# Optimization experiments

Measured on AMD Instinct MI355X. Metric: run time of the kernel, lower is better.

The kernel has to match this reference:

```python
import math
import jax, jax.numpy as jnp
import numpy as np

B, T, O, C, H, L, V = 4, 1024, 128, 512, 8, 6, 32000
HD = C // H
PAD_ID = 0
EPS = 1e-6  # flax LayerNorm default


def _logit(p):
    p = float(min(max(p, 1e-06), 1.0 - 1e-06))
    return math.log(p / (1.0 - p))


def _ln(x, scale, bias):
    m = jnp.mean(x, axis=-1, keepdims=True)
    v = jnp.mean(jnp.square(x - m), axis=-1, keepdims=True)
    return (x - m) * jax.lax.rsqrt(v + EPS) * scale + bias


def _rope(x, fc):
    b, t, h, d = x.shape
    xc = jax.lax.complex(x[..., 0::2], x[..., 1::2])
    xr = xc * fc
    return jnp.stack([xr.real, xr.imag], axis=-1).reshape(b, t, h, d)


def _freqs_cis(dim, max_len, theta=10000.0):
    freqs = 1.0 / theta ** (jnp.arange(0, dim, 2) / dim)
    t = jnp.arange(max_len)
    return jnp.exp(1j * jnp.outer(t, freqs))[None, :, None, :]


def setup_inputs() -> dict:
    key = jax.random.key(0)
    ks = iter(jax.random.split(key, 64))
    def w(shape, s=0.02):
        return jax.random.normal(next(ks), shape, jnp.float32) * s
    inp = {
        'tokens_w': jax.random.randint(next(ks), (B, T), 0, V, dtype=jnp.int32),
        'mem': w((B, O, C), 1.0),
        'ssum': w((B, C), 1.0),
        'embed': w((V, C)),
        'mem_adapter_w': w((C, C)), 'mem_adapter_b': jnp.zeros((C,), jnp.float32),
        'mem_norm_scale': jnp.ones((C,), jnp.float32), 'mem_norm_bias': jnp.zeros((C,), jnp.float32),
        'alpha_gate': jnp.full((C,), _logit(0.1), jnp.float32),
        'lambda_gate': jnp.full((C,), _logit(0.9), jnp.float32),
        'ssum_proj_w': w((C, C)),
        'ln1_scale': jnp.ones((L, C), jnp.float32), 'ln1_bias': jnp.zeros((L, C), jnp.float32),
        'lnkv_scale': jnp.ones((L, C), jnp.float32), 'lnkv_bias': jnp.zeros((L, C), jnp.float32),
        'q_w': w((L, C, C)), 'q_b': jnp.zeros((L, C), jnp.float32),
        'k_w': w((L, C, C)), 'k_b': jnp.zeros((L, C), jnp.float32),
        'v_w': w((L, C, C)), 'v_b': jnp.zeros((L, C), jnp.float32),
        'o_w': w((L, C, C)), 'o_b': jnp.zeros((L, C), jnp.float32),
        'ln2_scale': jnp.ones((L, C), jnp.float32), 'ln2_bias': jnp.zeros((L, C), jnp.float32),
        'mlp_w1': w((L, C, 4 * C)), 'mlp_b1': jnp.zeros((L, 4 * C), jnp.float32),
        'mlp_w2': w((L, 4 * C, C)), 'mlp_b2': jnp.zeros((L, C), jnp.float32),
        'final_ln_scale': jnp.ones((C,), jnp.float32), 'final_ln_bias': jnp.zeros((C,), jnp.float32),
        'out_w': w((C, V)), 'out_b': jnp.zeros((V,), jnp.float32),
    }
    return inp


def reference(tokens_w, mem, ssum, embed, mem_adapter_w, mem_adapter_b,
              mem_norm_scale, mem_norm_bias, alpha_gate, lambda_gate, ssum_proj_w,
              ln1_scale, ln1_bias, lnkv_scale, lnkv_bias,
              q_w, q_b, k_w, k_b, v_w, v_b, o_w, o_b,
              ln2_scale, ln2_bias, mlp_w1, mlp_b1, mlp_w2, mlp_b2,
              final_ln_scale, final_ln_bias, out_w, out_b):
    x = embed[tokens_w]  # [B,T,C]
    mem_p = _ln(mem @ mem_adapter_w + mem_adapter_b, mem_norm_scale, mem_norm_bias)  # [B,O,C]
    alpha = jax.nn.sigmoid(alpha_gate)
    x = x + (ssum @ ssum_proj_w)[:, None, :] * alpha[None, None, :]

    causal = jnp.tril(jnp.ones((T, T), bool))
    full_mask = jnp.concatenate([jnp.ones((T, O), bool), causal], axis=1)  # [T,T+O]
    valid_curr = tokens_w != PAD_ID
    valid_k = jnp.concatenate([jnp.ones((B, O), bool), valid_curr], axis=1)  # [B,T+O]
    mask = full_mask[None, None, :, :] & valid_k[:, None, None, :]  # [B,1,T,T+O]

    fc = _freqs_cis(HD, T + O + 10)
    f_q = fc[:, -T:, :, :]
    f_k = fc[:, -(T + O):, :, :]
    scale = 1.0 / math.sqrt(HD)

    cur = x
    for i in range(L):
        nx = _ln(cur, ln1_scale[i], ln1_bias[i])
        kv = jnp.concatenate([mem_p, cur], axis=1)  # [B,T+O,C]
        nkv = _ln(kv, lnkv_scale[i], lnkv_bias[i])
        q = (nx @ q_w[i] + q_b[i]).reshape(B, T, H, HD)
        k = (nkv @ k_w[i] + k_b[i]).reshape(B, T + O, H, HD)
        v = (nkv @ v_w[i] + v_b[i]).reshape(B, T + O, H, HD)
        q = _rope(q, f_q)
        k = _rope(k, f_k)
        scores = jnp.einsum('bqhd,bkhd->bhqk', q, k) * scale
        scores = jnp.where(mask, scores, -1e9)
        probs = jax.nn.softmax(scores, axis=-1)
        attn = jnp.einsum('bhqk,bkhd->bqhd', probs, v).reshape(B, T, C)
        cur = cur + attn @ o_w[i] + o_b[i]
        h = _ln(cur, ln2_scale[i], ln2_bias[i])
        h = jax.nn.gelu(h @ mlp_w1[i] + mlp_b1[i]) @ mlp_w2[i] + mlp_b2[i]
        cur = cur + h

    cur = _ln(cur, final_ln_scale, final_ln_bias)
    new_mem = cur[:, -O:, :]
    out_mask = valid_curr.astype(jnp.float32)[:, :, None]
    masked = cur * out_mask
    logits = masked @ out_w + out_b
    win_sum = jnp.sum(masked, axis=1) / (jnp.sum(out_mask, axis=1) + 1e-6)
    lam = jax.nn.sigmoid(lambda_gate)
    new_ssum = ssum * lam[None, :] + win_sum * (1.0 - lam[None, :])
    return (new_mem, new_ssum, logits)
```

## Files before the change

### kernel.cpp

```cpp
#include <hip/hip_runtime.h>
#include <math.h>

#define NB 4
#define NT 1024
#define NO 128
#define NC 512
#define NH 8
#define NL 6
#define NV 32000
#define NHD 64
#define NTK (NT + NO)
#define NFF (4 * NC)

__device__ __forceinline__ float sigmoidf_(float x) { return 1.f / (1.f + __expf(-x)); }
__device__ __forceinline__ float gelu_(float x) {
    const float k0 = 0.7978845608028654f;
    float x3 = x * x * x;
    return 0.5f * x * (1.f + tanhf(k0 * (x + 0.044715f * x3)));
}

template <int ACT>
__global__ __launch_bounds__(256) void gemm_kernel(
    const float* __restrict__ A, const float* __restrict__ W,
    const float* __restrict__ bias, const float* __restrict__ res,
    float* __restrict__ out, int M, int N, int K)
{
    __shared__ float As[16][65];
    __shared__ float Bs[16][65];
    int tid = threadIdx.x;
    int bm = blockIdx.y * 64, bn = blockIdx.x * 64;
    int tx = tid & 15, ty = tid >> 4;
    float acc[4][4];
#pragma unroll
    for (int i = 0; i < 4; i++)
#pragma unroll
        for (int j = 0; j < 4; j++) acc[i][j] = 0.f;

    for (int k0 = 0; k0 < K; k0 += 16) {
        int ak = tid & 15, am = tid >> 4;
#pragma unroll
        for (int r = 0; r < 4; r++) {
            int m = am + r * 16;
            int gm = bm + m;
            As[ak][m] = (gm < M) ? A[(size_t)gm * K + k0 + ak] : 0.f;
        }
        int wn = tid & 63, wk = tid >> 6;
#pragma unroll
        for (int r = 0; r < 4; r++) {
            int kk = wk + r * 4;
            Bs[kk][wn] = W[(size_t)(k0 + kk) * N + bn + wn];
        }
        __syncthreads();
#pragma unroll
        for (int kk = 0; kk < 16; kk++) {
            float a[4], b[4];
#pragma unroll
            for (int i = 0; i < 4; i++) a[i] = As[kk][ty * 4 + i];
#pragma unroll
            for (int j = 0; j < 4; j++) b[j] = Bs[kk][tx * 4 + j];
#pragma unroll
            for (int i = 0; i < 4; i++)
#pragma unroll
                for (int j = 0; j < 4; j++) acc[i][j] = fmaf(a[i], b[j], acc[i][j]);
        }
        __syncthreads();
    }

#pragma unroll
    for (int i = 0; i < 4; i++) {
        int gm = bm + ty * 4 + i;
        if (gm >= M) continue;
#pragma unroll
        for (int j = 0; j < 4; j++) {
            int gn = bn + tx * 4 + j;
            float v = acc[i][j];
            if (bias) v += bias[gn];
            if (ACT == 1) v = gelu_(v);
            if (res) v += res[(size_t)gm * N + gn];
            out[(size_t)gm * N + gn] = v;
        }
    }
}

__global__ __launch_bounds__(256) void ln_kernel(
    const float* __restrict__ x, float* __restrict__ y,
    const float* __restrict__ scale, const float* __restrict__ bias)
{
    int row = blockIdx.x, tid = threadIdx.x;
    const float* xr = x + (size_t)row * NC;
    float v0 = xr[tid], v1 = xr[tid + 256];
    __shared__ float red[256];
    red[tid] = v0 + v1;
    __syncthreads();
    for (int s = 128; s > 0; s >>= 1) { if (tid < s) red[tid] += red[tid + s]; __syncthreads(); }
    float mean = red[0] * (1.f / NC);
    __syncthreads();
    float d0 = v0 - mean, d1 = v1 - mean;
    red[tid] = d0 * d0 + d1 * d1;
    __syncthreads();
    for (int s = 128; s > 0; s >>= 1) { if (tid < s) red[tid] += red[tid + s]; __syncthreads(); }
    float rs = rsqrtf(red[0] * (1.f / NC) + 1e-6f);
    float* yr = y + (size_t)row * NC;
    yr[tid] = d0 * rs * scale[tid] + bias[tid];
    yr[tid + 256] = d1 * rs * scale[tid + 256] + bias[tid + 256];
}

__global__ __launch_bounds__(256) void lnkv_kernel(
    const float* __restrict__ mem_p, const float* __restrict__ cur,
    float* __restrict__ y, const float* __restrict__ scale, const float* __restrict__ bias)
{
    int row = blockIdx.x;
    int b = row / NTK, r = row % NTK;
    const float* xr = (r < NO) ? (mem_p + (size_t)(b * NO + r) * NC)
                               : (cur + (size_t)(b * NT + (r - NO)) * NC);
    int tid = threadIdx.x;
    float v0 = xr[tid], v1 = xr[tid + 256];
    __shared__ float red[256];
    red[tid] = v0 + v1;
    __syncthreads();
    for (int s = 128; s > 0; s >>= 1) { if (tid < s) red[tid] += red[tid + s]; __syncthreads(); }
    float mean = red[0] * (1.f / NC);
    __syncthreads();
    float d0 = v0 - mean, d1 = v1 - mean;
    red[tid] = d0 * d0 + d1 * d1;
    __syncthreads();
    for (int s = 128; s > 0; s >>= 1) { if (tid < s) red[tid] += red[tid + s]; __syncthreads(); }
    float rs = rsqrtf(red[0] * (1.f / NC) + 1e-6f);
    float* yr = y + (size_t)row * NC;
    yr[tid] = d0 * rs * scale[tid] + bias[tid];
    yr[tid + 256] = d1 * rs * scale[tid + 256] + bias[tid + 256];
}

__global__ __launch_bounds__(256) void embed_kernel(
    const int* __restrict__ tokens, const float* __restrict__ emb,
    const float* __restrict__ sp, const float* __restrict__ alpha_gate,
    float* __restrict__ cur)
{
    int idx = blockIdx.x * 256 + threadIdx.x;
    int c = idx & (NC - 1);
    int t = (idx >> 9) & (NT - 1);
    int b = idx >> 19;
    int tok = tokens[b * NT + t];
    float a = sigmoidf_(alpha_gate[c]);
    cur[idx] = emb[(size_t)tok * NC + c] + sp[b * NC + c] * a;
}

__global__ __launch_bounds__(256) void rope_kernel(float* __restrict__ x, int rows, int pos_off)
{
    int idx = blockIdx.x * 256 + threadIdx.x;
    int total = NB * rows * NH * 32;
    if (idx >= total) return;
    int j = idx & 31;
    int h = (idx >> 5) & 7;
    int r = (idx >> 8) % rows;
    int b = (idx >> 8) / rows;
    double freq = exp(-(2.0 * j / 64.0) * log(10000.0));
    double ang = (double)(r + pos_off) * freq;
    double sd, cd;
    sincos(ang, &sd, &cd);
    float s = (float)sd, c = (float)cd;
    size_t base = (size_t)((b * rows + r) * NH + h) * NHD + 2 * j;
    float x0 = x[base], x1 = x[base + 1];
    x[base] = x0 * c - x1 * s;
    x[base + 1] = x0 * s + x1 * c;
}

__global__ __launch_bounds__(256) void attn_kernel(
    const float* __restrict__ q, const float* __restrict__ k,
    const float* __restrict__ v, const int* __restrict__ tokens,
    float* __restrict__ attn)
{
    __shared__ float qs[8][NHD];
    __shared__ float sc[8][NTK];
    __shared__ float red[256];
    int tid = threadIdx.x;
    int qt = blockIdx.x;
    int h = blockIdx.y;
    int b = blockIdx.z;
    int t0 = qt * 8;

    for (int idx = tid; idx < 8 * NHD; idx += 256) {
        int qi = idx >> 6, d = idx & 63;
        qs[qi][d] = q[(size_t)(b * NT + t0 + qi) * NC + h * NHD + d];
    }
    __syncthreads();

    const float scale = 0.125f;
    int lk = tid & 31, qi = tid >> 5;
    int t = t0 + qi;
    for (int it = 0; it < NTK / 32; it++) {
        int kk = it * 32 + lk;
        const float* krow = k + (size_t)(b * NTK + kk) * NC + h * NHD;
        const float4* k4 = reinterpret_cast<const float4*>(krow);
        float s = 0.f;
#pragma unroll
        for (int d4 = 0; d4 < 16; d4++) {
            float4 kv = k4[d4];
            s = fmaf(qs[qi][d4 * 4 + 0], kv.x, s);
            s = fmaf(qs[qi][d4 * 4 + 1], kv.y, s);
            s = fmaf(qs[qi][d4 * 4 + 2], kv.z, s);
            s = fmaf(qs[qi][d4 * 4 + 3], kv.w, s);
        }
        bool valid;
        if (kk < NO) {
            valid = true;
        } else {
            int tkidx = kk - NO;
            valid = (tkidx <= t) && (tokens[b * NT + tkidx] != 0);
        }
        sc[qi][kk] = valid ? s * scale : -1e9f;
    }
    __syncthreads();

    for (int r = 0; r < 8; r++) {
        float m = -3e38f;
        for (int kk = tid; kk < NTK; kk += 256) m = fmaxf(m, sc[r][kk]);
        red[tid] = m;
        __syncthreads();
        for (int s = 128; s > 0; s >>= 1) { if (tid < s) red[tid] = fmaxf(red[tid], red[tid + s]); __syncthreads(); }
        m = red[0];
        __syncthreads();
        float ss = 0.f;
        for (int kk = tid; kk < NTK; kk += 256) {
            float e = __expf(sc[r][kk] - m);
            sc[r][kk] = e;
            ss += e;
        }
        red[tid] = ss;
        __syncthreads();
        for (int s = 128; s > 0; s >>= 1) { if (tid < s) red[tid] += red[tid + s]; __syncthreads(); }
        float inv = 1.f / red[0];
        __syncthreads();
        for (int kk = tid; kk < NTK; kk += 256) sc[r][kk] *= inv;
        __syncthreads();
    }

    int d = tid & 63, g = tid >> 6;
    int q0 = g * 2, q1 = g * 2 + 1;
    float a0 = 0.f, a1 = 0.f;
    for (int kk = 0; kk < NTK; kk++) {
        float vv = v[(size_t)(b * NTK + kk) * NC + h * NHD + d];
        a0 = fmaf(sc[q0][kk], vv, a0);
        a1 = fmaf(sc[q1][kk], vv, a1);
    }
    attn[(size_t)(b * NT + t0 + q0) * NC + h * NHD + d] = a0;
    attn[(size_t)(b * NT + t0 + q1) * NC + h * NHD + d] = a1;
}

__global__ __launch_bounds__(256) void newmem_kernel(const float* __restrict__ fin, float* __restrict__ out)
{
    int idx = blockIdx.x * 256 + threadIdx.x;
    int c = idx & 511;
    int o = (idx >> 9) & 127;
    int b = idx >> 16;
    out[idx] = fin[(size_t)(b * NT + (NT - NO) + o) * NC + c];
}

__global__ __launch_bounds__(256) void masked_kernel(
    const float* __restrict__ fin, const int* __restrict__ tokens, float* __restrict__ out)
{
    int idx = blockIdx.x * 256 + threadIdx.x;
    int t = (idx >> 9) & (NT - 1);
    int b = idx >> 19;
    out[idx] = (tokens[b * NT + t] != 0) ? fin[idx] : 0.f;
}

__global__ __launch_bounds__(256) void ssum_kernel(
    const float* __restrict__ masked, const int* __restrict__ tokens,
    const float* __restrict__ ssum_in, const float* __restrict__ lambda_gate,
    float* __restrict__ out)
{
    int idx = blockIdx.x * 256 + threadIdx.x;
    int c = idx & 511;
    int b = idx >> 9;
    float sum = 0.f, cnt = 0.f;
    for (int t = 0; t < NT; t++) {
        sum += masked[(size_t)(b * NT + t) * NC + c];
        cnt += (tokens[b * NT + t] != 0) ? 1.f : 0.f;
    }
    float lam = sigmoidf_(lambda_gate[c]);
    out[idx] = ssum_in[idx] * lam + (sum / (cnt + 1e-6f)) * (1.f - lam);
}

extern "C" void kernel_launch(void* const* d_in, const int* in_sizes, int n_in,
                              void* d_out, int out_size, void* d_ws, size_t ws_size,
                              hipStream_t stream)
{
    const int* tokens          = (const int*)d_in[0];
    const float* mem           = (const float*)d_in[1];
    const float* ssum          = (const float*)d_in[2];
    const float* embedw        = (const float*)d_in[3];
    const float* mem_adapter_w = (const float*)d_in[4];
    const float* mem_adapter_b = (const float*)d_in[5];
    const float* mem_norm_s    = (const float*)d_in[6];
    const float* mem_norm_b    = (const float*)d_in[7];
    const float* alpha_gate    = (const float*)d_in[8];
    const float* lambda_gate   = (const float*)d_in[9];
    const float* ssum_proj_w   = (const float*)d_in[10];
    const float* ln1_scale     = (const float*)d_in[11];
    const float* ln1_bias      = (const float*)d_in[12];
    const float* lnkv_scale    = (const float*)d_in[13];
    const float* lnkv_bias     = (const float*)d_in[14];
    const float* q_w           = (const float*)d_in[15];
    const float* q_b           = (const float*)d_in[16];
    const float* k_w           = (const float*)d_in[17];
    const float* k_b           = (const float*)d_in[18];
    const float* v_w           = (const float*)d_in[19];
    const float* v_b           = (const float*)d_in[20];
    const float* o_w           = (const float*)d_in[21];
    const float* o_b           = (const float*)d_in[22];
    const float* ln2_scale     = (const float*)d_in[23];
    const float* ln2_bias      = (const float*)d_in[24];
    const float* mlp_w1        = (const float*)d_in[25];
    const float* mlp_b1        = (const float*)d_in[26];
    const float* mlp_w2        = (const float*)d_in[27];
    const float* mlp_b2        = (const float*)d_in[28];
    const float* final_ln_s    = (const float*)d_in[29];
    const float* final_ln_b    = (const float*)d_in[30];
    const float* out_w         = (const float*)d_in[31];
    const float* out_b         = (const float*)d_in[32];

    float* w = (float*)d_ws;
    float* cur   = w;
    float* nx    = cur + NB * NT * NC;
    float* mem_p = nx + NB * NT * NC;
    float* nkv   = mem_p + NB * NO * NC;
    float* big   = nkv + NB * NTK * NC;
    float* qb = big;
    float* kb = qb + NB * NT * NC;
    float* vb = kb + NB * NTK * NC;
    float* ab = vb + NB * NTK * NC;
    float* mlph    = big;
    float* maskedb = big;
    float* spb     = big;
    float* memtmp  = nkv;

    float* out_mem    = (float*)d_out;
    float* out_ssum   = out_mem + NB * NO * NC;
    float* out_logits = out_ssum + NB * NC;

    gemm_kernel<0><<<dim3(NC / 64, 1), 256, 0, stream>>>(ssum, ssum_proj_w, nullptr, nullptr, spb, NB, NC, NC);
    embed_kernel<<<(NB * NT * NC) / 256, 256, 0, stream>>>(tokens, embedw, spb, alpha_gate, cur);
    gemm_kernel<0><<<dim3(NC / 64, (NB * NO) / 64), 256, 0, stream>>>(mem, mem_adapter_w, mem_adapter_b, nullptr, memtmp, NB * NO, NC, NC);
    ln_kernel<<<NB * NO, 256, 0, stream>>>(memtmp, mem_p, mem_norm_s, mem_norm_b);

    for (int l = 0; l < NL; l++) {
        const float* qw = q_w + (size_t)l * NC * NC;
        const float* kw = k_w + (size_t)l * NC * NC;
        const float* vw = v_w + (size_t)l * NC * NC;
        const float* ow = o_w + (size_t)l * NC * NC;
        const float* w1 = mlp_w1 + (size_t)l * NC * NFF;
        const float* w2 = mlp_w2 + (size_t)l * NFF * NC;

        ln_kernel<<<NB * NT, 256, 0, stream>>>(cur, nx, ln1_scale + l * NC, ln1_bias + l * NC);
        lnkv_kernel<<<NB * NTK, 256, 0, stream>>>(mem_p, cur, nkv, lnkv_scale + l * NC, lnkv_bias + l * NC);
        gemm_kernel<0><<<dim3(NC / 64, NB * NT / 64), 256, 0, stream>>>(nx, qw, q_b + l * NC, nullptr, qb, NB * NT, NC, NC);
        gemm_kernel<0><<<dim3(NC / 64, NB * NTK / 64), 256, 0, stream>>>(nkv, kw, k_b + l * NC, nullptr, kb, NB * NTK, NC, NC);
        gemm_kernel<0><<<dim3(NC / 64, NB * NTK / 64), 256, 0, stream>>>(nkv, vw, v_b + l * NC, nullptr, vb, NB * NTK, NC, NC);
        rope_kernel<<<(NB * NT * NH * 32) / 256, 256, 0, stream>>>(qb, NT, NO + 10);
        rope_kernel<<<(NB * NTK * NH * 32) / 256, 256, 0, stream>>>(kb, NTK, 10);
        attn_kernel<<<dim3(NT / 8, NH, NB), 256, 0, stream>>>(qb, kb, vb, tokens, ab);
        gemm_kernel<0><<<dim3(NC / 64, NB * NT / 64), 256, 0, stream>>>(ab, ow, o_b + l * NC, cur, cur, NB * NT, NC, NC);
        ln_kernel<<<NB * NT, 256, 0, stream>>>(cur, nx, ln2_scale + l * NC, ln2_bias + l * NC);
        gemm_kernel<1><<<dim3(NFF / 64, NB * NT / 64), 256, 0, stream>>>(nx, w1, mlp_b1 + l * NFF, nullptr, mlph, NB * NT, NFF, NC);
        gemm_kernel<0><<<dim3(NC / 64, NB * NT / 64), 256, 0, stream>>>(mlph, w2, mlp_b2 + l * NC, cur, cur, NB * NT, NC, NFF);
    }

    ln_kernel<<<NB * NT, 256, 0, stream>>>(cur, nx, final_ln_s, final_ln_b);
    newmem_kernel<<<(NB * NO * NC) / 256, 256, 0, stream>>>(nx, out_mem);
    masked_kernel<<<(NB * NT * NC) / 256, 256, 0, stream>>>(nx, tokens, maskedb);
    ssum_kernel<<<(NB * NC) / 256, 256, 0, stream>>>(maskedb, tokens, ssum, lambda_gate, out_ssum);
    gemm_kernel<0><<<dim3(NV / 64, NB * NT / 64), 256, 0, stream>>>(maskedb, out_w, out_b, nullptr, out_logits, NB * NT, NV, NC);
}
```

Measured before the change: 16.58 ms.

## Use 128x128 GEMM tiles with 8x8 register blocking and rework attention softmax/PV

Each GEMM block now computes a 128x128 output tile: every thread holds an 8x8 accumulator, global loads use float4, and LDS reads are vectorised. This raises arithmetic intensity per byte of shared and global memory, and all launch grids are resized to match. The attention kernel replaces the block-wide LDS tree reductions in softmax with per-wave shuffle reductions and defers the normalisation to the output. It also stages V tiles in LDS so they are reused across the query rows. The trade-off is higher register pressure, which may lower occupancy, and fewer blocks for the small GEMMs.

```diff
diff --git a/kernel.cpp b/kernel.cpp
--- a/kernel.cpp
+++ b/kernel.cpp
@@ -25,54 +25,71 @@
     const float* __restrict__ bias, const float* __restrict__ res,
     float* __restrict__ out, int M, int N, int K)
 {
-    __shared__ float As[16][65];
-    __shared__ float Bs[16][65];
+    __shared__ float As[16][132];
+    __shared__ float Bs[16][132];
     int tid = threadIdx.x;
-    int bm = blockIdx.y * 64, bn = blockIdx.x * 64;
+    int bm = blockIdx.y * 128, bn = blockIdx.x * 128;
     int tx = tid & 15, ty = tid >> 4;
-    float acc[4][4];
-#pragma unroll
-    for (int i = 0; i < 4; i++)
-#pragma unroll
-        for (int j = 0; j < 4; j++) acc[i][j] = 0.f;
+    float acc[8][8];
+#pragma unroll
+    for (int i = 0; i < 8; i++)
+#pragma unroll
+        for (int j = 0; j < 8; j++) acc[i][j] = 0.f;
+
+    int arow = tid >> 2, akq = (tid & 3) * 4;
+    int bn4 = (tid & 31) * 4, bkk = tid >> 5;
 
     for (int k0 = 0; k0 < K; k0 += 16) {
-        int ak = tid & 15, am = tid >> 4;
-#pragma unroll
-        for (int r = 0; r < 4; r++) {
-            int m = am + r * 16;
-            int gm = bm + m;
-            As[ak][m] = (gm < M) ? A[(size_t)gm * K + k0 + ak] : 0.f;
-        }
-        int wn = tid & 63, wk = tid >> 6;
-#pragma unroll
-        for (int r = 0; r < 4; r++) {
-            int kk = wk + r * 4;
-            Bs[kk][wn] = W[(size_t)(k0 + kk) * N + bn + wn];
+        float4 a4[2];
+#pragma unroll
+        for (int r = 0; r < 2; r++) {
+            int gm = bm + arow + 64 * r;
+            if (gm < M) a4[r] = *reinterpret_cast<const float4*>(A + (size_t)gm * K + k0 + akq);
+            else        a4[r] = make_float4(0.f, 0.f, 0.f, 0.f);
+        }
+        float4 b4[2];
+#pragma unroll
+        for (int r = 0; r < 2; r++) {
+            int kk = bkk + 8 * r;
+            b4[r] = *reinterpret_cast<const float4*>(W + (size_t)(k0 + kk) * N + bn + bn4);
+        }
+#pragma unroll
+        for (int r = 0; r < 2; r++) {
+            int m = arow + 64 * r;
+            As[akq + 0][m] = a4[r].x;
+            As[akq + 1][m] = a4[r].y;
+            As[akq + 2][m] = a4[r].z;
+            As[akq + 3][m] = a4[r].w;
+        }
+#pragma unroll
+        for (int r = 0; r < 2; r++) {
+            *reinterpret_cast<float4*>(&Bs[bkk + 8 * r][bn4]) = b4[r];
         }
         __syncthreads();
 #pragma unroll
         for (int kk = 0; kk < 16; kk++) {
-            float a[4], b[4];
-#pragma unroll
-            for (int i = 0; i < 4; i++) a[i] = As[kk][ty * 4 + i];
-#pragma unroll
-            for (int j = 0; j < 4; j++) b[j] = Bs[kk][tx * 4 + j];
-#pragma unroll
-            for (int i = 0; i < 4; i++)
-#pragma unroll
-                for (int j = 0; j < 4; j++) acc[i][j] = fmaf(a[i], b[j], acc[i][j]);
+            float a[8], b[8];
+            *reinterpret_cast<float4*>(&a[0]) = *reinterpret_cast<const float4*>(&As[kk][ty * 4]);
+            *reinterpret_cast<float4*>(&a[4]) = *reinterpret_cast<const float4*>(&As[kk][ty * 4 + 64]);
+            *reinterpret_cast<float4*>(&b[0]) = *reinterpret_cast<const float4*>(&Bs[kk][tx * 4]);
+            *reinterpret_cast<float4*>(&b[4]) = *reinterpret_cast<const float4*>(&Bs[kk][tx * 4 + 64]);
+#pragma unroll
+            for (int i = 0; i < 8; i++)
+#pragma unroll
+                for (int j = 0; j < 8; j++) acc[i][j] = fmaf(a[i], b[j], acc[i][j]);
         }
         __syncthreads();
     }
 
 #pragma unroll
-    for (int i = 0; i < 4; i++) {
-        int gm = bm + ty * 4 + i;
+    for (int i = 0; i < 8; i++) {
+        int m = ty * 4 + (i & 3) + ((i & 4) ? 64 : 0);
+        int gm = bm + m;
         if (gm >= M) continue;
 #pragma unroll
-        for (int j = 0; j < 4; j++) {
-            int gn = bn + tx * 4 + j;
+        for (int j = 0; j < 8; j++) {
+            int n = tx * 4 + (j & 3) + ((j & 4) ? 64 : 0);
+            int gn = bn + n;
             float v = acc[i][j];
             if (bias) v += bias[gn];
             if (ACT == 1) v = gelu_(v);
@@ -172,7 +189,7 @@
 {
     __shared__ float qs[8][NHD];
     __shared__ float sc[8][NTK];
-    __shared__ float red[256];
+    __shared__ float vs[32][68];
     int tid = threadIdx.x;
     int qt = blockIdx.x;
     int h = blockIdx.y;
@@ -186,65 +203,84 @@
     __syncthreads();
 
     const float scale = 0.125f;
-    int lk = tid & 31, qi = tid >> 5;
-    int t = t0 + qi;
-    for (int it = 0; it < NTK / 32; it++) {
-        int kk = it * 32 + lk;
-        const float* krow = k + (size_t)(b * NTK + kk) * NC + h * NHD;
-        const float4* k4 = reinterpret_cast<const float4*>(krow);
-        float s = 0.f;
-#pragma unroll
-        for (int d4 = 0; d4 < 16; d4++) {
-            float4 kv = k4[d4];
-            s = fmaf(qs[qi][d4 * 4 + 0], kv.x, s);
-            s = fmaf(qs[qi][d4 * 4 + 1], kv.y, s);
-            s = fmaf(qs[qi][d4 * 4 + 2], kv.z, s);
-            s = fmaf(qs[qi][d4 * 4 + 3], kv.w, s);
-        }
-        bool valid;
-        if (kk < NO) {
-            valid = true;
-        } else {
-            int tkidx = kk - NO;
-            valid = (tkidx <= t) && (tokens[b * NT + tkidx] != 0);
-        }
-        sc[qi][kk] = valid ? s * scale : -1e9f;
-    }
-    __syncthreads();
-
-    for (int r = 0; r < 8; r++) {
-        float m = -3e38f;
-        for (int kk = tid; kk < NTK; kk += 256) m = fmaxf(m, sc[r][kk]);
-        red[tid] = m;
+    {
+        int lk = tid & 31, qi = tid >> 5;
+        int t = t0 + qi;
+        for (int it = 0; it < NTK / 32; it++) {
+            int kk = it * 32 + lk;
+            const float4* k4 = reinterpret_cast<const float4*>(k + (size_t)(b * NTK + kk) * NC + h * NHD);
+            float s = 0.f;
+#pragma unroll
+            for (int d4 = 0; d4 < 16; d4++) {
+                float4 kv = k4[d4];
+                s = fmaf(qs[qi][d4 * 4 + 0], kv.x, s);
+                s = fmaf(qs[qi][d4 * 4 + 1], kv.y, s);
+                s = fmaf(qs[qi][d4 * 4 + 2], kv.z, s);
+                s = fmaf(qs[qi][d4 * 4 + 3], kv.w, s);
+            }
+            bool valid;
+            if (kk < NO) {
+                valid = true;
+            } else {
+                int tk = kk - NO;
+                valid = (tk <= t) && (tokens[b * NT + tk] != 0);
+            }
+            sc[qi][kk] = valid ? s * scale : -1e9f;
+        }
+    }
+    __syncthreads();
+
+    int lane = tid & 63, w = tid >> 6;
+    float invs[2];
+#pragma unroll
+    for (int rr = 0; rr < 2; rr++) {
+        int r = 2 * w + rr;
+        float e[18];
+        float m = -3.0e38f;
+#pragma unroll
+        for (int c = 0; c < 18; c++) { e[c] = sc[r][c * 64 + lane]; m = fmaxf(m, e[c]); }
+#pragma unroll
+        for (int s = 32; s > 0; s >>= 1) m = fmaxf(m, __shfl_xor(m, s));
+        float ssum = 0.f;
+#pragma unroll
+        for (int c = 0; c < 18; c++) {
+            float ev = __expf(e[c] - m);
+            sc[r][c * 64 + lane] = ev;
+            ssum += ev;
+        }
+#pragma unroll
+        for (int s = 32; s > 0; s >>= 1) ssum += __shfl_xor(ssum, s);
+        invs[rr] = 1.f / ssum;
+    }
+
+    float a0 = 0.f, a1 = 0.f;
+    int r0 = 2 * w, r1 = 2 * w + 1;
+    int vkk = tid >> 3, vdB = (tid & 7) * 8;
+    for (int kt = 0; kt < NTK / 32; kt++) {
+        const float* vrow = v + (size_t)(b * NTK + kt * 32 + vkk) * NC + h * NHD + vdB;
+        float4 va = *reinterpret_cast<const float4*>(vrow);
+        float4 vb = *reinterpret_cast<const float4*>(vrow + 4);
         __syncthreads();
-        for (int s = 128; s > 0; s >>= 1) { if (tid < s) red[tid] = fmaxf(red[tid], red[tid + s]); __syncthreads(); }
-        m = red[0];
+        *reinterpret_cast<float4*>(&vs[vkk][vdB]) = va;
+        *reinterpret_cast<float4*>(&vs[vkk][vdB + 4]) = vb;
         __syncthreads();
-        float ss = 0.f;
-        for (int kk = tid; kk < NTK; kk += 256) {
-            float e = __expf(sc[r][kk] - m);
-            sc[r][kk] = e;
-            ss += e;
-        }
-        red[tid] = ss;
-        __syncthreads();
-        for (int s = 128; s > 0; s >>= 1) { if (tid < s) red[tid] += red[tid + s]; __syncthreads(); }
-        float inv = 1.f / red[0];
-        __syncthreads();
-        for (int kk = tid; kk < NTK; kk += 256) sc[r][kk] *= inv;
-        __syncthreads();
-    }
-
-    int d = tid & 63, g = tid >> 6;
-    int q0 = g * 2, q1 = g * 2 + 1;
-    float a0 = 0.f, a1 = 0.f;
-    for (int kk = 0; kk < NTK; kk++) {
-        float vv = v[(size_t)(b * NTK + kk) * NC + h * NHD + d];
-        a0 = fmaf(sc[q0][kk], vv, a0);
-        a1 = fmaf(sc[q1][kk], vv, a1);
-    }
-    attn[(size_t)(b * NT + t0 + q0) * NC + h * NHD + d] = a0;
-    attn[(size_t)(b * NT + t0 + q1) * NC + h * NHD + d] = a1;
+        const float4* p0 = reinterpret_cast<const float4*>(&sc[r0][kt * 32]);
+        const float4* p1 = reinterpret_cast<const float4*>(&sc[r1][kt * 32]);
+#pragma unroll
+        for (int k4 = 0; k4 < 8; k4++) {
+            float4 e0 = p0[k4], e1 = p1[k4];
+            float v0 = vs[k4 * 4 + 0][lane];
+            float v1 = vs[k4 * 4 + 1][lane];
+            float v2 = vs[k4 * 4 + 2][lane];
+            float v3 = vs[k4 * 4 + 3][lane];
+            a0 = fmaf(e0.x, v0, a0); a1 = fmaf(e1.x, v0, a1);
+            a0 = fmaf(e0.y, v1, a0); a1 = fmaf(e1.y, v1, a1);
+            a0 = fmaf(e0.z, v2, a0); a1 = fmaf(e1.z, v2, a1);
+            a0 = fmaf(e0.w, v3, a0); a1 = fmaf(e1.w, v3, a1);
+        }
+    }
+    attn[(size_t)(b * NT + t0 + r0) * NC + h * NHD + lane] = a0 * invs[0];
+    attn[(size_t)(b * NT + t0 + r1) * NC + h * NHD + lane] = a1 * invs[1];
 }
 
 __global__ __launch_bounds__(256) void newmem_kernel(const float* __restrict__ fin, float* __restrict__ out)
@@ -339,9 +375,9 @@
     float* out_ssum   = out_mem + NB * NO * NC;
     float* out_logits = out_ssum + NB * NC;
 
-    gemm_kernel<0><<<dim3(NC / 64, 1), 256, 0, stream>>>(ssum, ssum_proj_w, nullptr, nullptr, spb, NB, NC, NC);
+    gemm_kernel<0><<<dim3(NC / 128, 1), 256, 0, stream>>>(ssum, ssum_proj_w, nullptr, nullptr, spb, NB, NC, NC);
     embed_kernel<<<(NB * NT * NC) / 256, 256, 0, stream>>>(tokens, embedw, spb, alpha_gate, cur);
-    gemm_kernel<0><<<dim3(NC / 64, (NB * NO) / 64), 256, 0, stream>>>(mem, mem_adapter_w, mem_adapter_b, nullptr, memtmp, NB * NO, NC, NC);
+    gemm_kernel<0><<<dim3(NC / 128, (NB * NO) / 128), 256, 0, stream>>>(mem, mem_adapter_w, mem_adapter_b, nullptr, memtmp, NB * NO, NC, NC);
     ln_kernel<<<NB * NO, 256, 0, stream>>>(memtmp, mem_p, mem_norm_s, mem_norm_b);
 
     for (int l = 0; l < NL; l++) {
@@ -354,21 +390,21 @@
 
         ln_kernel<<<NB * NT, 256, 0, stream>>>(cur, nx, ln1_scale + l * NC, ln1_bias + l * NC);
         lnkv_kernel<<<NB * NTK, 256, 0, stream>>>(mem_p, cur, nkv, lnkv_scale + l * NC, lnkv_bias + l * NC);
-        gemm_kernel<0><<<dim3(NC / 64, NB * NT / 64), 256, 0, stream>>>(nx, qw, q_b + l * NC, nullptr, qb, NB * NT, NC, NC);
-        gemm_kernel<0><<<dim3(NC / 64, NB * NTK / 64), 256, 0, stream>>>(nkv, kw, k_b + l * NC, nullptr, kb, NB * NTK, NC, NC);
-        gemm_kernel<0><<<dim3(NC / 64, NB * NTK / 64), 256, 0, stream>>>(nkv, vw, v_b + l * NC, nullptr, vb, NB * NTK, NC, NC);
+        gemm_kernel<0><<<dim3(NC / 128, NB * NT / 128), 256, 0, stream>>>(nx, qw, q_b + l * NC, nullptr, qb, NB * NT, NC, NC);
+        gemm_kernel<0><<<dim3(NC / 128, NB * NTK / 128), 256, 0, stream>>>(nkv, kw, k_b + l * NC, nullptr, kb, NB * NTK, NC, NC);
+        gemm_kernel<0><<<dim3(NC / 128, NB * NTK / 128), 256, 0, stream>>>(nkv, vw, v_b + l * NC, nullptr, vb, NB * NTK, NC, NC);
         rope_kernel<<<(NB * NT * NH * 32) / 256, 256, 0, stream>>>(qb, NT, NO + 10);
         rope_kernel<<<(NB * NTK * NH * 32) / 256, 256, 0, stream>>>(kb, NTK, 10);
         attn_kernel<<<dim3(NT / 8, NH, NB), 256, 0, stream>>>(qb, kb, vb, tokens, ab);
-        gemm_kernel<0><<<dim3(NC / 64, NB * NT / 64), 256, 0, stream>>>(ab, ow, o_b + l * NC, cur, cur, NB * NT, NC, NC);
+        gemm_kernel<0><<<dim3(NC / 128, NB * NT / 128), 256, 0, stream>>>(ab, ow, o_b + l * NC, cur, cur, NB * NT, NC, NC);
         ln_kernel<<<NB * NT, 256, 0, stream>>>(cur, nx, ln2_scale + l * NC, ln2_bias + l * NC);
-        gemm_kernel<1><<<dim3(NFF / 64, NB * NT / 64), 256, 0, stream>>>(nx, w1, mlp_b1 + l * NFF, nullptr, mlph, NB * NT, NFF, NC);
-        gemm_kernel<0><<<dim3(NC / 64, NB * NT / 64), 256, 0, stream>>>(mlph, w2, mlp_b2 + l * NC, cur, cur, NB * NT, NC, NFF);
+        gemm_kernel<1><<<dim3(NFF / 128, NB * NT / 128), 256, 0, stream>>>(nx, w1, mlp_b1 + l * NFF, nullptr, mlph, NB * NT, NFF, NC);
+        gemm_kernel<0><<<dim3(NC / 128, NB * NT / 128), 256, 0, stream>>>(mlph, w2, mlp_b2 + l * NC, cur, cur, NB * NT, NC, NFF);
     }
 
     ln_kernel<<<NB * NT, 256, 0, stream>>>(cur, nx, final_ln_s, final_ln_b);
     newmem_kernel<<<(NB * NO * NC) / 256, 256, 0, stream>>>(nx, out_mem);
     masked_kernel<<<(NB * NT * NC) / 256, 256, 0, stream>>>(nx, tokens, maskedb);
     ssum_kernel<<<(NB * NC) / 256, 256, 0, stream>>>(maskedb, tokens, ssum, lambda_gate, out_ssum);
-    gemm_kernel<0><<<dim3(NV / 64, NB * NT / 64), 256, 0, stream>>>(maskedb, out_w, out_b, nullptr, out_logits, NB * NT, NV, NC);
-}
+    gemm_kernel<0><<<dim3(NV / 128, NB * NT / 128), 256, 0, stream>>>(maskedb, out_w, out_b, nullptr, out_logits, NB * NT, NV, NC);
+}
```

After: 14.00 ms. 1.18x faster.
